# Kernel optimization log

Hardware: AMD Instinct MI355X
Metric: run time of the kernel (lower is better)

## Reference

```python
import jax, jax.numpy as jnp
import numpy as np

B, V, N, Y, HID, T = 512, 16, 8192, 32, 512, 8


def setup_inputs() -> dict:
    key = jax.random.key(0)
    ks = jax.random.split(key, 16)
    tables = jax.random.randint(ks[0], (B, V, N), 0, Y, dtype=jnp.int64 if jax.config.jax_enable_x64 else jnp.int32)
    sigma = jax.random.randint(ks[1], (B, N), 0, Y, dtype=tables.dtype)
    base_obs = jax.random.randint(ks[2], (B,), 0, Y, dtype=tables.dtype)
    actions = jax.random.randint(ks[3], (B, T), 0, V, dtype=tables.dtype)
    responses = jax.random.randint(ks[4], (B, T), 0, Y, dtype=tables.dtype)
    s = 0.02
    W1 = jax.random.normal(ks[5], (Y + V + 4, HID), jnp.float32) * s
    b1 = jnp.zeros((HID,), jnp.float32)
    W2 = jax.random.normal(ks[6], (HID, V), jnp.float32) * s
    b2 = jnp.zeros((V,), jnp.float32)
    Wy1 = jax.random.normal(ks[7], (Y + V, HID), jnp.float32) * s
    by1 = jnp.zeros((HID,), jnp.float32)
    Wy2 = jax.random.normal(ks[8], (HID, Y), jnp.float32) * s
    by2 = jnp.zeros((Y,), jnp.float32)
    return {"tables": tables, "sigma": sigma, "base_obs": base_obs,
            "actions": actions, "responses": responses, "t": T,
            "W1": W1, "b1": b1, "W2": W2, "b2": b2,
            "Wy1": Wy1, "by1": by1, "Wy2": Wy2, "by2": by2}


def _predict_y(tables, sigma, base_obs, actions, responses, t,
               W1, b1, W2, b2, Wy1, by1, Wy2, by2):
    Bb, Vv, Nn = tables.shape
    Yy = Wy2.shape[1]
    # --- state_dist: boolean mask accumulation over t steps (vectorized) ---
    m = tables[:, 0, :] == base_obs[:, None]                       # [B,N]
    if t > 0:
        lbl = jnp.take_along_axis(tables, actions[:, :t, None], axis=1)  # [B,t,N]
        m = m & (lbl == responses[:, :t, None]).all(axis=1)
    w = m.astype(jnp.float32)
    denom = jnp.clip(w.sum(axis=-1, keepdims=True), 1.0)
    state_dist = w / denom                                          # [B,N]
    # --- sigma_dist: weighted histogram of sigma labels ---
    p_sig = jnp.zeros((Bb, Yy), jnp.float32).at[
        jnp.arange(Bb)[:, None], sigma].add(state_dist)             # [B,Y]
    # --- unique label count per view over candidate states (fused histogram) ---
    cand = (state_dist > 0.0).astype(jnp.float32)                   # [B,N]
    hist = jnp.zeros((Bb, Vv, Yy), jnp.float32).at[
        jnp.arange(Bb)[:, None, None], jnp.arange(Vv)[None, :, None], tables
    ].add(cand[:, None, :])                                         # [B,V,Y]
    uniq = (hist > 0.0).sum(axis=-1).astype(jnp.float32)            # [B,V]
    # --- entropy / topk / mass features ---
    pc = jnp.clip(p_sig, 1e-9)
    ent = -(pc * jnp.log(pc)).sum(axis=-1, keepdims=True)           # [B,1]
    top2 = jax.lax.top_k(p_sig, 2)[0]                               # [B,2]
    mass = state_dist.max(axis=-1, keepdims=True)                   # [B,1]
    feat = jnp.concatenate([p_sig, uniq, ent, top2[:, 0:1], top2[:, 1:2], mass], axis=-1)
    # --- z_mlp ---
    h = jax.nn.gelu(feat @ W1 + b1, approximate=False)
    z_logits = h @ W2 + b2                                          # [B,V]
    # --- straight-through one-hot z ---
    z_soft = jax.nn.softmax(z_logits, axis=-1)
    z_hard = jax.nn.one_hot(jnp.argmax(z_soft, axis=-1), Vv, dtype=z_soft.dtype)
    z = z_hard - jax.lax.stop_gradient(z_soft) + z_soft
    # --- y_head ---
    fy = jnp.concatenate([p_sig, z], axis=-1)
    hy = jax.nn.gelu(fy @ Wy1 + by1, approximate=False)
    return hy @ Wy2 + by2                                           # [B,Y]


def reference(tables, sigma, base_obs, actions, responses, t,
              W1, b1, W2, b2, Wy1, by1, Wy2, by2):
    return _predict_y(tables, sigma, base_obs, actions, responses, int(t),
                      W1, b1, W2, b2, Wy1, by1, Wy2, by2)
```

## Files before the change

kernel.cpp:

```cpp
#include <hip/hip_runtime.h>
#include <math.h>

#define BB 512
#define VV 16
#define NN 8192
#define YY 32
#define HID 512
#define TT 8
#define NTHR 1024

__device__ __forceinline__ float gelu_exact(float x) {
    return x * 0.5f * (1.0f + erff(x * 0.70710678118654752440f));
}

__device__ __forceinline__ int parse_t(const unsigned* p) {
    unsigned w0 = p[0];
    if (w0 >= 1u && w0 <= 64u) return (int)w0;
    if (w0 == 0u) {
        unsigned w1 = p[1];
        if (w1 == 0u) return 0;
        double d = __hiloint2double((int)w1, (int)w0);
        if (d >= 0.0 && d <= 64.0 && d == floor(d)) return (int)d;
        return 0;
    }
    float f = __uint_as_float(w0);
    if (f >= 0.0f && f <= 64.0f && f == floorf(f)) return (int)f;
    return TT;
}

__global__ __launch_bounds__(NTHR) void fused_model_kernel(
    const int* __restrict__ tables, const int* __restrict__ sigma,
    const int* __restrict__ base_obs, const int* __restrict__ actions,
    const int* __restrict__ responses, const unsigned* __restrict__ tptr,
    const float* __restrict__ W1, const float* __restrict__ b1,
    const float* __restrict__ W2, const float* __restrict__ b2,
    const float* __restrict__ Wy1, const float* __restrict__ by1,
    const float* __restrict__ Wy2, const float* __restrict__ by2,
    float* __restrict__ out)
{
    const int b = blockIdx.x;
    const int tid = threadIdx.x;

    __shared__ int      s_cnt_sig[YY];
    __shared__ unsigned s_labmask[VV];
    __shared__ int      s_count;
    __shared__ float    s_feat[52];
    __shared__ float    s_h[HID];
    __shared__ float    s_part[HID];
    __shared__ float    s_fy[YY + VV];
    __shared__ float    s_logits[VV];
    __shared__ int      s_act[TT], s_resp[TT];
    __shared__ int      s_t;

    if (tid < YY) s_cnt_sig[tid] = 0;
    if (tid < VV) s_labmask[tid] = 0u;
    if (tid == 0) { s_count = 0; int t = parse_t(tptr); s_t = t > TT ? TT : t; }
    if (tid < TT) { s_act[tid] = actions[b * TT + tid]; s_resp[tid] = responses[b * TT + tid]; }
    __syncthreads();

    const int  base    = base_obs[b];
    const int  t       = s_t;
    const long rowbase = (long)b * VV * NN;

    {
        const int n0 = tid * 8;
        const int4* tp = (const int4*)(tables + rowbase + n0);
        int4 x0 = tp[0], x1 = tp[1];
        int vals[8] = { x0.x, x0.y, x0.z, x0.w, x1.x, x1.y, x1.z, x1.w };
        #pragma unroll
        for (int s = 0; s < 8; ++s) {
            if (vals[s] == base) {
                const int n = n0 + s;
                bool ok = true;
                for (int j = 0; j < t; ++j)
                    if (tables[rowbase + s_act[j] * NN + n] != s_resp[j]) { ok = false; break; }
                if (ok) {
                    atomicAdd(&s_count, 1);
                    atomicAdd(&s_cnt_sig[sigma[(long)b * NN + n] & 31], 1);
                    #pragma unroll
                    for (int v = 0; v < VV; ++v)
                        atomicOr(&s_labmask[v], 1u << (tables[rowbase + v * NN + n] & 31));
                }
            }
        }
    }
    __syncthreads();

    if (tid < YY) {
        int cnt = s_count;
        float inv = 1.0f / (cnt > 0 ? (float)cnt : 1.0f);
        float p = (float)s_cnt_sig[tid] * inv;
        s_feat[tid] = p;
        float et = p > 0.0f ? -p * logf(p) : 0.0f;
        float t1 = p, t2 = -1e30f;
        #pragma unroll
        for (int off = 1; off < 32; off <<= 1) {
            float oe = __shfl_xor(et, off, 32);
            float o1 = __shfl_xor(t1, off, 32);
            float o2 = __shfl_xor(t2, off, 32);
            et += oe;
            float hi = fmaxf(t1, o1);
            float lo = fminf(t1, o1);
            t2 = fmaxf(lo, fmaxf(t2, o2));
            t1 = hi;
        }
        if (tid == 0) {
            s_feat[48] = et;
            s_feat[49] = t1;
            s_feat[50] = t2;
            s_feat[51] = cnt > 0 ? inv : 0.0f;
        }
    }
    if (tid < VV) s_feat[YY + tid] = (float)__popc(s_labmask[tid]);
    __syncthreads();

    if (tid < HID) {
        float acc = b1[tid];
        #pragma unroll
        for (int k = 0; k < 52; ++k) acc += s_feat[k] * W1[k * HID + tid];
        s_h[tid] = gelu_exact(acc);
    }
    __syncthreads();

    if (tid < HID) {
        const int o = tid & 15, kc = tid >> 4;
        float acc = 0.0f;
        #pragma unroll
        for (int q = 0; q < 16; ++q) {
            const int k = kc * 16 + q;
            acc += s_h[k] * W2[k * VV + o];
        }
        s_part[tid] = acc;
    }
    __syncthreads();
    if (tid < VV) {
        float acc = b2[tid];
        for (int kc = 0; kc < 32; ++kc) acc += s_part[kc * 16 + tid];
        s_logits[tid] = acc;
    }
    __syncthreads();

    if (tid == 0) {
        float mx = s_logits[0]; int am = 0;
        for (int o = 1; o < VV; ++o) if (s_logits[o] > mx) { mx = s_logits[o]; am = o; }
        float sum = 0.0f;
        float e[VV];
        #pragma unroll
        for (int o = 0; o < VV; ++o) { e[o] = expf(s_logits[o] - mx); sum += e[o]; }
        float isum = 1.0f / sum;
        #pragma unroll
        for (int o = 0; o < VV; ++o) {
            float soft = e[o] * isum;
            s_fy[YY + o] = ((o == am ? 1.0f : 0.0f) - soft) + soft;
        }
    }
    if (tid < YY) s_fy[tid] = s_feat[tid];
    __syncthreads();

    if (tid < HID) {
        float acc = by1[tid];
        #pragma unroll
        for (int k = 0; k < 48; ++k) acc += s_fy[k] * Wy1[k * HID + tid];
        s_h[tid] = gelu_exact(acc);
    }
    __syncthreads();

    if (tid < HID) {
        const int o = tid & 31, kc = tid >> 5;
        float acc = 0.0f;
        #pragma unroll
        for (int q = 0; q < 32; ++q) {
            const int k = kc * 32 + q;
            acc += s_h[k] * Wy2[k * YY + o];
        }
        s_part[tid] = acc;
    }
    __syncthreads();
    if (tid < YY) {
        float acc = by2[tid];
        for (int kc = 0; kc < 16; ++kc) acc += s_part[kc * 32 + tid];
        out[b * YY + tid] = acc;
    }
}

extern "C" void kernel_launch(void* const* d_in, const int* in_sizes, int n_in,
                              void* d_out, int out_size, void* d_ws, size_t ws_size,
                              hipStream_t stream) {
    const void *tables = nullptr, *sigma = nullptr, *tptr = nullptr;
    const void *W1 = nullptr, *W2 = nullptr, *Wy1 = nullptr, *Wy2 = nullptr;
    const void *b2 = nullptr, *by2 = nullptr;
    const void* amb512[3] = { nullptr, nullptr, nullptr }; int n512 = 0;
    const void* amb4096[2] = { nullptr, nullptr };         int n4096 = 0;

    for (int i = 0; i < n_in; ++i) {
        switch (in_sizes[i]) {
            case 67108864: tables = d_in[i]; break;
            case 4194304:  sigma  = d_in[i]; break;
            case 26624:    W1     = d_in[i]; break;
            case 8192:     W2     = d_in[i]; break;
            case 24576:    Wy1    = d_in[i]; break;
            case 16384:    Wy2    = d_in[i]; break;
            case 16:       b2     = d_in[i]; break;
            case 32:       by2    = d_in[i]; break;
            case 1:        tptr   = d_in[i]; break;
            case 4096:     if (n4096 < 2) amb4096[n4096++] = d_in[i]; break;
            case 512:      if (n512  < 3) amb512[n512++]   = d_in[i]; break;
            default: break;
        }
    }

    const void* base_obs  = amb512[0];
    const void* b1        = amb512[1];
    const void* by1       = amb512[2];
    const void* actions   = amb4096[0];
    const void* responses = amb4096[1];

    fused_model_kernel<<<BB, NTHR, 0, stream>>>(
        (const int*)tables, (const int*)sigma,
        (const int*)base_obs, (const int*)actions, (const int*)responses,
        (const unsigned*)tptr,
        (const float*)W1, (const float*)b1,
        (const float*)W2, (const float*)b2,
        (const float*)Wy1, (const float*)by1,
        (const float*)Wy2, (const float*)by2,
        (float*)d_out);
}
```

Measured before the change: 25.86 us.

## Split feature extraction and batched MLP into two kernels

The single fused kernel is split in two. The first computes the per-row features and writes them to workspace. The second runs the MLP heads on groups of 8 batch rows per block, so each weight load is reused across 8 rows instead of being reloaded by every block. The cost is an extra kernel launch, a round trip through global memory for the features, and fewer blocks in the MLP stage.

```diff
diff --git a/kernel.cpp b/kernel.cpp
--- a/kernel.cpp
+++ b/kernel.cpp
@@ -8,6 +8,8 @@
 #define HID 512
 #define TT 8
 #define NTHR 1024
+#define GB 8
+#define NBLK_B (BB / GB)
 
 __device__ __forceinline__ float gelu_exact(float x) {
     return x * 0.5f * (1.0f + erff(x * 0.70710678118654752440f));
@@ -28,15 +30,11 @@
     return TT;
 }
 
-__global__ __launch_bounds__(NTHR) void fused_model_kernel(
+__global__ __launch_bounds__(NTHR) void feat_kernel(
     const int* __restrict__ tables, const int* __restrict__ sigma,
     const int* __restrict__ base_obs, const int* __restrict__ actions,
     const int* __restrict__ responses, const unsigned* __restrict__ tptr,
-    const float* __restrict__ W1, const float* __restrict__ b1,
-    const float* __restrict__ W2, const float* __restrict__ b2,
-    const float* __restrict__ Wy1, const float* __restrict__ by1,
-    const float* __restrict__ Wy2, const float* __restrict__ by2,
-    float* __restrict__ out)
+    float* __restrict__ feat_ws)
 {
     const int b = blockIdx.x;
     const int tid = threadIdx.x;
@@ -45,10 +43,6 @@
     __shared__ unsigned s_labmask[VV];
     __shared__ int      s_count;
     __shared__ float    s_feat[52];
-    __shared__ float    s_h[HID];
-    __shared__ float    s_part[HID];
-    __shared__ float    s_fy[YY + VV];
-    __shared__ float    s_logits[VV];
     __shared__ int      s_act[TT], s_resp[TT];
     __shared__ int      s_t;
 
@@ -114,72 +108,125 @@
     if (tid < VV) s_feat[YY + tid] = (float)__popc(s_labmask[tid]);
     __syncthreads();
 
-    if (tid < HID) {
-        float acc = b1[tid];
-        #pragma unroll
-        for (int k = 0; k < 52; ++k) acc += s_feat[k] * W1[k * HID + tid];
-        s_h[tid] = gelu_exact(acc);
-    }
-    __syncthreads();
-
-    if (tid < HID) {
+    if (tid < 52) feat_ws[b * 52 + tid] = s_feat[tid];
+}
+
+__global__ __launch_bounds__(HID) void mlp_kernel(
+    const float* __restrict__ feat_ws,
+    const float* __restrict__ W1, const float* __restrict__ b1,
+    const float* __restrict__ W2, const float* __restrict__ b2,
+    const float* __restrict__ Wy1, const float* __restrict__ by1,
+    const float* __restrict__ Wy2, const float* __restrict__ by2,
+    float* __restrict__ out)
+{
+    const int g0  = blockIdx.x * GB;
+    const int tid = threadIdx.x;
+
+    __shared__ float s_feat[GB][52];
+    __shared__ float s_h[GB][HID];
+    __shared__ float s_part[HID][GB];
+    __shared__ float s_fy[GB][YY + VV];
+    __shared__ float s_logits[GB][VV];
+
+    for (int i = tid; i < GB * 52; i += HID) s_feat[i / 52][i % 52] = feat_ws[g0 * 52 + i];
+    __syncthreads();
+
+    {
+        float acc[GB];
+        const float bv = b1[tid];
+        #pragma unroll
+        for (int g = 0; g < GB; ++g) acc[g] = bv;
+        for (int k = 0; k < 52; ++k) {
+            const float wv = W1[k * HID + tid];
+            #pragma unroll
+            for (int g = 0; g < GB; ++g) acc[g] += s_feat[g][k] * wv;
+        }
+        #pragma unroll
+        for (int g = 0; g < GB; ++g) s_h[g][tid] = gelu_exact(acc[g]);
+    }
+    __syncthreads();
+
+    {
         const int o = tid & 15, kc = tid >> 4;
-        float acc = 0.0f;
+        float acc[GB];
+        #pragma unroll
+        for (int g = 0; g < GB; ++g) acc[g] = 0.0f;
         #pragma unroll
         for (int q = 0; q < 16; ++q) {
             const int k = kc * 16 + q;
-            acc += s_h[k] * W2[k * VV + o];
-        }
-        s_part[tid] = acc;
-    }
-    __syncthreads();
-    if (tid < VV) {
-        float acc = b2[tid];
-        for (int kc = 0; kc < 32; ++kc) acc += s_part[kc * 16 + tid];
-        s_logits[tid] = acc;
-    }
-    __syncthreads();
-
-    if (tid == 0) {
-        float mx = s_logits[0]; int am = 0;
-        for (int o = 1; o < VV; ++o) if (s_logits[o] > mx) { mx = s_logits[o]; am = o; }
+            const float wv = W2[k * VV + o];
+            #pragma unroll
+            for (int g = 0; g < GB; ++g) acc[g] += s_h[g][k] * wv;
+        }
+        #pragma unroll
+        for (int g = 0; g < GB; ++g) s_part[tid][g] = acc[g];
+    }
+    __syncthreads();
+    if (tid < VV * GB) {
+        const int o = tid & 15, g = tid >> 4;
+        float acc = b2[o];
+        for (int kc = 0; kc < 32; ++kc) acc += s_part[kc * 16 + o][g];
+        s_logits[g][o] = acc;
+    }
+    __syncthreads();
+
+    if (tid < GB) {
+        const int g = tid;
+        float mx = s_logits[g][0]; int am = 0;
+        for (int o = 1; o < VV; ++o) if (s_logits[g][o] > mx) { mx = s_logits[g][o]; am = o; }
         float sum = 0.0f;
         float e[VV];
         #pragma unroll
-        for (int o = 0; o < VV; ++o) { e[o] = expf(s_logits[o] - mx); sum += e[o]; }
+        for (int o = 0; o < VV; ++o) { e[o] = expf(s_logits[g][o] - mx); sum += e[o]; }
         float isum = 1.0f / sum;
         #pragma unroll
         for (int o = 0; o < VV; ++o) {
             float soft = e[o] * isum;
-            s_fy[YY + o] = ((o == am ? 1.0f : 0.0f) - soft) + soft;
-        }
-    }
-    if (tid < YY) s_fy[tid] = s_feat[tid];
-    __syncthreads();
-
-    if (tid < HID) {
-        float acc = by1[tid];
-        #pragma unroll
-        for (int k = 0; k < 48; ++k) acc += s_fy[k] * Wy1[k * HID + tid];
-        s_h[tid] = gelu_exact(acc);
-    }
-    __syncthreads();
-
-    if (tid < HID) {
+            s_fy[g][YY + o] = ((o == am ? 1.0f : 0.0f) - soft) + soft;
+        }
+    }
+    if (tid < YY * GB) {
+        const int y = tid & 31, g = tid >> 5;
+        s_fy[g][y] = s_feat[g][y];
+    }
+    __syncthreads();
+
+    {
+        float acc[GB];
+        const float bv = by1[tid];
+        #pragma unroll
+        for (int g = 0; g < GB; ++g) acc[g] = bv;
+        for (int k = 0; k < 48; ++k) {
+            const float wv = Wy1[k * HID + tid];
+            #pragma unroll
+            for (int g = 0; g < GB; ++g) acc[g] += s_fy[g][k] * wv;
+        }
+        #pragma unroll
+        for (int g = 0; g < GB; ++g) s_h[g][tid] = gelu_exact(acc[g]);
+    }
+    __syncthreads();
+
+    {
         const int o = tid & 31, kc = tid >> 5;
-        float acc = 0.0f;
+        float acc[GB];
+        #pragma unroll
+        for (int g = 0; g < GB; ++g) acc[g] = 0.0f;
         #pragma unroll
         for (int q = 0; q < 32; ++q) {
             const int k = kc * 32 + q;
-            acc += s_h[k] * Wy2[k * YY + o];
-        }
-        s_part[tid] = acc;
-    }
-    __syncthreads();
-    if (tid < YY) {
-        float acc = by2[tid];
-        for (int kc = 0; kc < 16; ++kc) acc += s_part[kc * 32 + tid];
-        out[b * YY + tid] = acc;
+            const float wv = Wy2[k * YY + o];
+            #pragma unroll
+            for (int g = 0; g < GB; ++g) acc[g] += s_h[g][k] * wv;
+        }
+        #pragma unroll
+        for (int g = 0; g < GB; ++g) s_part[tid][g] = acc[g];
+    }
+    __syncthreads();
+    if (tid < YY * GB) {
+        const int o = tid & 31, g = tid >> 5;
+        float acc = by2[o];
+        for (int kc = 0; kc < 16; ++kc) acc += s_part[kc * 32 + o][g];
+        out[(g0 + g) * YY + o] = acc;
     }
 }
 
@@ -215,10 +262,15 @@
     const void* actions   = amb4096[0];
     const void* responses = amb4096[1];
 
-    fused_model_kernel<<<BB, NTHR, 0, stream>>>(
+    float* feat_ws = (float*)d_ws;
+
+    feat_kernel<<<BB, NTHR, 0, stream>>>(
         (const int*)tables, (const int*)sigma,
         (const int*)base_obs, (const int*)actions, (const int*)responses,
-        (const unsigned*)tptr,
+        (const unsigned*)tptr, feat_ws);
+
+    mlp_kernel<<<NBLK_B, HID, 0, stream>>>(
+        feat_ws,
         (const float*)W1, (const float*)b1,
         (const float*)W2, (const float*)b2,
         (const float*)Wy1, (const float*)by1,
```

Result: slower. 77.72 us (+200.5%).

## Process two batch rows per block with 512 threads each

Applied to the files above, without the earlier changes.

Each 1024-thread block now handles two batch rows, with each half of the block working on one row. Each thread scans 16 table entries instead of 8, and all MLP stages keep every thread busy instead of idling half the block. This halves the grid to 256 blocks, fewer than one per CU on the 256-CU MI355X, and gives each thread more serial work in the table scan, which may reduce latency hiding.

```diff
diff --git a/kernel.cpp b/kernel.cpp
--- a/kernel.cpp
+++ b/kernel.cpp
@@ -7,6 +7,8 @@
 #define YY 32
 #define HID 512
 #define TT 8
+#define GB 2
+#define NBLK (BB / GB)
 #define NTHR 1024
 
 __device__ __forceinline__ float gelu_exact(float x) {
@@ -38,24 +40,27 @@
     const float* __restrict__ Wy2, const float* __restrict__ by2,
     float* __restrict__ out)
 {
-    const int b = blockIdx.x;
     const int tid = threadIdx.x;
-
-    __shared__ int      s_cnt_sig[YY];
-    __shared__ unsigned s_labmask[VV];
-    __shared__ int      s_count;
-    __shared__ float    s_feat[52];
-    __shared__ float    s_h[HID];
-    __shared__ float    s_part[HID];
-    __shared__ float    s_fy[YY + VV];
-    __shared__ float    s_logits[VV];
-    __shared__ int      s_act[TT], s_resp[TT];
+    const int g   = tid >> 9;
+    const int lt  = tid & 511;
+    const int b   = blockIdx.x * GB + g;
+
+    __shared__ int      s_cnt_sig[GB][YY];
+    __shared__ unsigned s_labmask[GB][VV];
+    __shared__ int      s_count[GB];
+    __shared__ float    s_feat[GB][52];
+    __shared__ float    s_h[GB][HID];
+    __shared__ float    s_part[GB][HID];
+    __shared__ float    s_fy[GB][YY + VV];
+    __shared__ float    s_logits[GB][VV];
+    __shared__ int      s_act[GB][TT], s_resp[GB][TT];
     __shared__ int      s_t;
 
-    if (tid < YY) s_cnt_sig[tid] = 0;
-    if (tid < VV) s_labmask[tid] = 0u;
-    if (tid == 0) { s_count = 0; int t = parse_t(tptr); s_t = t > TT ? TT : t; }
-    if (tid < TT) { s_act[tid] = actions[b * TT + tid]; s_resp[tid] = responses[b * TT + tid]; }
+    if (tid < GB * YY) s_cnt_sig[tid >> 5][tid & 31] = 0;
+    if (tid < GB * VV) s_labmask[tid >> 4][tid & 15] = 0u;
+    if (tid < GB) s_count[tid] = 0;
+    if (tid == 0) { int t = parse_t(tptr); s_t = t > TT ? TT : t; }
+    if (lt < TT) { s_act[g][lt] = actions[b * TT + lt]; s_resp[g][lt] = responses[b * TT + lt]; }
     __syncthreads();
 
     const int  base    = base_obs[b];
@@ -63,34 +68,36 @@
     const long rowbase = (long)b * VV * NN;
 
     {
-        const int n0 = tid * 8;
+        const int n0 = lt * 16;
         const int4* tp = (const int4*)(tables + rowbase + n0);
-        int4 x0 = tp[0], x1 = tp[1];
-        int vals[8] = { x0.x, x0.y, x0.z, x0.w, x1.x, x1.y, x1.z, x1.w };
-        #pragma unroll
-        for (int s = 0; s < 8; ++s) {
+        int4 x0 = tp[0], x1 = tp[1], x2 = tp[2], x3 = tp[3];
+        int vals[16] = { x0.x, x0.y, x0.z, x0.w, x1.x, x1.y, x1.z, x1.w,
+                         x2.x, x2.y, x2.z, x2.w, x3.x, x3.y, x3.z, x3.w };
+        #pragma unroll
+        for (int s = 0; s < 16; ++s) {
             if (vals[s] == base) {
                 const int n = n0 + s;
                 bool ok = true;
                 for (int j = 0; j < t; ++j)
-                    if (tables[rowbase + s_act[j] * NN + n] != s_resp[j]) { ok = false; break; }
+                    if (tables[rowbase + s_act[g][j] * NN + n] != s_resp[g][j]) { ok = false; break; }
                 if (ok) {
-                    atomicAdd(&s_count, 1);
-                    atomicAdd(&s_cnt_sig[sigma[(long)b * NN + n] & 31], 1);
+                    atomicAdd(&s_count[g], 1);
+                    atomicAdd(&s_cnt_sig[g][sigma[(long)b * NN + n] & 31], 1);
                     #pragma unroll
                     for (int v = 0; v < VV; ++v)
-                        atomicOr(&s_labmask[v], 1u << (tables[rowbase + v * NN + n] & 31));
+                        atomicOr(&s_labmask[g][v], 1u << (tables[rowbase + v * NN + n] & 31));
                 }
             }
         }
     }
     __syncthreads();
 
-    if (tid < YY) {
-        int cnt = s_count;
+    if (tid < GB * YY) {
+        const int gg = tid >> 5, y = tid & 31;
+        int cnt = s_count[gg];
         float inv = 1.0f / (cnt > 0 ? (float)cnt : 1.0f);
-        float p = (float)s_cnt_sig[tid] * inv;
-        s_feat[tid] = p;
+        float p = (float)s_cnt_sig[gg][y] * inv;
+        s_feat[gg][y] = p;
         float et = p > 0.0f ? -p * logf(p) : 0.0f;
         float t1 = p, t2 = -1e30f;
         #pragma unroll
@@ -104,82 +111,91 @@
             t2 = fmaxf(lo, fmaxf(t2, o2));
             t1 = hi;
         }
-        if (tid == 0) {
-            s_feat[48] = et;
-            s_feat[49] = t1;
-            s_feat[50] = t2;
-            s_feat[51] = cnt > 0 ? inv : 0.0f;
-        }
-    }
-    if (tid < VV) s_feat[YY + tid] = (float)__popc(s_labmask[tid]);
-    __syncthreads();
-
-    if (tid < HID) {
-        float acc = b1[tid];
-        #pragma unroll
-        for (int k = 0; k < 52; ++k) acc += s_feat[k] * W1[k * HID + tid];
-        s_h[tid] = gelu_exact(acc);
-    }
-    __syncthreads();
-
-    if (tid < HID) {
-        const int o = tid & 15, kc = tid >> 4;
+        if (y == 0) {
+            s_feat[gg][48] = et;
+            s_feat[gg][49] = t1;
+            s_feat[gg][50] = t2;
+            s_feat[gg][51] = cnt > 0 ? inv : 0.0f;
+        }
+    }
+    if (tid < GB * VV) {
+        const int gg = tid >> 4, v = tid & 15;
+        s_feat[gg][YY + v] = (float)__popc(s_labmask[gg][v]);
+    }
+    __syncthreads();
+
+    {
+        float acc = b1[lt];
+        #pragma unroll
+        for (int k = 0; k < 52; ++k) acc += s_feat[g][k] * W1[k * HID + lt];
+        s_h[g][lt] = gelu_exact(acc);
+    }
+    __syncthreads();
+
+    {
+        const int o = lt & 15, kc = lt >> 4;
         float acc = 0.0f;
         #pragma unroll
         for (int q = 0; q < 16; ++q) {
             const int k = kc * 16 + q;
-            acc += s_h[k] * W2[k * VV + o];
-        }
-        s_part[tid] = acc;
-    }
-    __syncthreads();
-    if (tid < VV) {
-        float acc = b2[tid];
-        for (int kc = 0; kc < 32; ++kc) acc += s_part[kc * 16 + tid];
-        s_logits[tid] = acc;
-    }
-    __syncthreads();
-
-    if (tid == 0) {
-        float mx = s_logits[0]; int am = 0;
-        for (int o = 1; o < VV; ++o) if (s_logits[o] > mx) { mx = s_logits[o]; am = o; }
+            acc += s_h[g][k] * W2[k * VV + o];
+        }
+        s_part[g][lt] = acc;
+    }
+    __syncthreads();
+    if (tid < GB * VV) {
+        const int gg = tid >> 4, o = tid & 15;
+        float acc = b2[o];
+        for (int kc = 0; kc < 32; ++kc) acc += s_part[gg][kc * 16 + o];
+        s_logits[gg][o] = acc;
+    }
+    __syncthreads();
+
+    if (tid < GB) {
+        const int gg = tid;
+        float mx = s_logits[gg][0]; int am = 0;
+        for (int o = 1; o < VV; ++o) if (s_logits[gg][o] > mx) { mx = s_logits[gg][o]; am = o; }
         float sum = 0.0f;
         float e[VV];
         #pragma unroll
-        for (int o = 0; o < VV; ++o) { e[o] = expf(s_logits[o] - mx); sum += e[o]; }
+        for (int o = 0; o < VV; ++o) { e[o] = expf(s_logits[gg][o] - mx); sum += e[o]; }
         float isum = 1.0f / sum;
         #pragma unroll
         for (int o = 0; o < VV; ++o) {
             float soft = e[o] * isum;
-            s_fy[YY + o] = ((o == am ? 1.0f : 0.0f) - soft) + soft;
-        }
-    }
-    if (tid < YY) s_fy[tid] = s_feat[tid];
-    __syncthreads();
-
-    if (tid < HID) {
-        float acc = by1[tid];
-        #pragma unroll
-        for (int k = 0; k < 48; ++k) acc += s_fy[k] * Wy1[k * HID + tid];
-        s_h[tid] = gelu_exact(acc);
-    }
-    __syncthreads();
-
-    if (tid < HID) {
-        const int o = tid & 31, kc = tid >> 5;
+            s_fy[gg][YY + o] = ((o == am ? 1.0f : 0.0f) - soft) + soft;
+        }
+    }
+    if (tid < GB * YY) {
+        const int gg = tid >> 5, y = tid & 31;
+        s_fy[gg][y] = s_feat[gg][y];
+    }
+    __syncthreads();
+
+    {
+        float acc = by1[lt];
+        #pragma unroll
+        for (int k = 0; k < 48; ++k) acc += s_fy[g][k] * Wy1[k * HID + lt];
+        s_h[g][lt] = gelu_exact(acc);
+    }
+    __syncthreads();
+
+    {
+        const int o = lt & 31, kc = lt >> 5;
         float acc = 0.0f;
         #pragma unroll
         for (int q = 0; q < 32; ++q) {
             const int k = kc * 32 + q;
-            acc += s_h[k] * Wy2[k * YY + o];
-        }
-        s_part[tid] = acc;
-    }
-    __syncthreads();
-    if (tid < YY) {
-        float acc = by2[tid];
-        for (int kc = 0; kc < 16; ++kc) acc += s_part[kc * 32 + tid];
-        out[b * YY + tid] = acc;
+            acc += s_h[g][k] * Wy2[k * YY + o];
+        }
+        s_part[g][lt] = acc;
+    }
+    __syncthreads();
+    if (tid < GB * YY) {
+        const int gg = tid >> 5, o = tid & 31;
+        float acc = by2[o];
+        for (int kc = 0; kc < 16; ++kc) acc += s_part[gg][kc * 32 + o];
+        out[(blockIdx.x * GB + gg) * YY + o] = acc;
     }
 }
 
@@ -215,7 +231,7 @@
     const void* actions   = amb4096[0];
     const void* responses = amb4096[1];
 
-    fused_model_kernel<<<BB, NTHR, 0, stream>>>(
+    fused_model_kernel<<<NBLK, NTHR, 0, stream>>>(
         (const int*)tables, (const int*)sigma,
         (const int*)base_obs, (const int*)actions, (const int*)responses,
         (const unsigned*)tptr,
```

Result: faster. 23.62 us, median of 2 (-8.7%).
